# Performance work log

Hardware: AMD Instinct MI355X
Metric: run time of the kernel (lower is better)

Reference implementation:

```python
import jax, jax.numpy as jnp
import numpy as np
import math

B, I, O = 512, 512, 512
MEXHAT_NORM = 2.0 / (math.sqrt(3.0) * math.pi ** 0.25)
BN_EPS = 1e-5


def setup_inputs() -> dict:
    key = jax.random.key(0)
    kx, kw = jax.random.split(key, 2)
    x = jax.random.normal(kx, (B, I), dtype=jnp.float32)
    scale = jnp.ones((I, O), dtype=jnp.float32)
    bias = jnp.zeros((I, O), dtype=jnp.float32)
    # kaiming_uniform_ with a=sqrt(5): bound = sqrt(6 / ((1 + a^2) * fan_in)) = 1/sqrt(fan_in)
    bound = 1.0 / math.sqrt(I)
    weight = jax.random.uniform(kw, (I, O), dtype=jnp.float32, minval=-bound, maxval=bound)
    # BatchNorm1d affine params
    gamma = jnp.ones((O,), dtype=jnp.float32)
    beta = jnp.zeros((O,), dtype=jnp.float32)
    return {"x": x, "scale": scale, "bias": bias, "weight": weight,
            "gamma": gamma, "beta": beta}


def _mexhat_kan(x, scale, bias, weight):
    # x: (B, I); scale/bias/weight: (I, O)
    t = (x[:, :, None] - bias[None, :, :]) / scale[None, :, :]      # (B, I, O)
    t2 = t * t
    wav = MEXHAT_NORM * (t2 - 1.0) * jnp.exp(-0.5 * t2)             # Mexican hat
    return jnp.einsum('bio,io->bo', wav, weight)                    # reduce over in_features


def _batchnorm_train(y, gamma, beta):
    # BatchNorm1d in training mode: biased batch statistics over the batch dim
    mean = jnp.mean(y, axis=0)
    var = jnp.mean((y - mean) ** 2, axis=0)
    return (y - mean) * jax.lax.rsqrt(var + BN_EPS) * gamma + beta


def reference(x, scale, bias, weight, gamma, beta):
    y = _mexhat_kan(x, scale, bias, weight)   # (B, O)
    return _batchnorm_train(y, gamma, beta)
```

## Files before the change

kernel.cpp:

```cpp
#include <hip/hip_runtime.h>
#include <math.h>

#define B_ 512
#define I_ 512
#define O_ 512
#define BO_ (B_*O_)

#define TB 64
#define TO 16
#define KI 16
#define ZN 8
#define NIZ (I_/ZN)
#define NCHZ (NIZ/KI)
#define LXS (TB + 4)

#define SQH    0.84932180028801904f
#define MN_   (-1.2023679775792928f)
#define NN_   (-0.86732507058407750f)
#define NORM_  (0.86732507058407750f)
#define K_EXP  (-0.72134752044448170f)
#define BN_EPS (1e-5f)
#define NCH (I_/KI)

#if defined(__has_builtin)
#if __has_builtin(__builtin_amdgcn_exp2f)
#define EXP2F(v) __builtin_amdgcn_exp2f(v)
#endif
#endif
#ifndef EXP2F
#define EXP2F(v) exp2f(v)
#endif

__global__ __launch_bounds__(256) void kanZ(
    const float* __restrict__ x, const float* __restrict__ scale,
    const float* __restrict__ bias, const float* __restrict__ weight,
    float* __restrict__ pY)
{
    __shared__ float Lx[KI][LXS];
    __shared__ float Lp[KI][TO][4];

    const int fid = blockIdx.x;
    const int xcd = fid & 7;
    const int seq = fid >> 3;
    const int ot  = xcd * 4 + (seq & 3);
    const int by  = (seq >> 2) & 7;
    const int iz  = seq >> 5;

    const int o0 = ot * TO;
    const int b0 = by * TB;
    const int z0 = iz * NIZ;

    const int t   = threadIdx.x;
    const int to  = t & (TO - 1);
    const int tb4 = t >> 4;
    const int lb  = t >> 2;
    const int lq  = t & 3;
    const int li  = t >> 4;
    const int lo  = t & 15;

    float acc0 = 0.f, acc1 = 0.f, acc2 = 0.f, acc3 = 0.f;

    for (int ch = 0; ch < NCHZ; ++ch) {
        const int i0 = z0 + ch * KI;
        const float4 xv = *reinterpret_cast<const float4*>(
            &x[(size_t)(b0 + lb) * I_ + i0 + lq * 4]);
        const int pidx = (i0 + li) * O_ + o0 + lo;
        const float sc = scale[pidx];
        const float bi = bias[pidx];
        const float w  = weight[pidx];

        __syncthreads();
        Lx[lq * 4 + 0][lb] = xv.x;
        Lx[lq * 4 + 1][lb] = xv.y;
        Lx[lq * 4 + 2][lb] = xv.z;
        Lx[lq * 4 + 3][lb] = xv.w;
        const float c = SQH * __builtin_amdgcn_rcpf(sc);
        Lp[li][lo][0] = c;
        Lp[li][lo][1] = -bi * c;
        Lp[li][lo][2] = MN_ * w;
        Lp[li][lo][3] = NN_ * w;
        __syncthreads();

        #pragma unroll
        for (int ii = 0; ii < KI; ++ii) {
            const float4 p  = *reinterpret_cast<const float4*>(&Lp[ii][to][0]);
            const float4 x4 = *reinterpret_cast<const float4*>(&Lx[ii][tb4 * 4]);
            {
                const float h  = fmaf(x4.x, p.x, p.y);
                const float un = -h * h;
                const float e  = EXP2F(un);
                const float gg = fmaf(un, p.z, p.w);
                acc0 = fmaf(gg, e, acc0);
            }
            {
                const float h  = fmaf(x4.y, p.x, p.y);
                const float un = -h * h;
                const float e  = EXP2F(un);
                const float gg = fmaf(un, p.z, p.w);
                acc1 = fmaf(gg, e, acc1);
            }
            {
                const float h  = fmaf(x4.z, p.x, p.y);
                const float un = -h * h;
                const float e  = EXP2F(un);
                const float gg = fmaf(un, p.z, p.w);
                acc2 = fmaf(gg, e, acc2);
            }
            {
                const float h  = fmaf(x4.w, p.x, p.y);
                const float un = -h * h;
                const float e  = EXP2F(un);
                const float gg = fmaf(un, p.z, p.w);
                acc3 = fmaf(gg, e, acc3);
            }
        }
    }

    const size_t base = ((size_t)iz * B_ + b0 + tb4 * 4) * O_ + o0 + to;
    pY[base + 0 * O_] = acc0;
    pY[base + 1 * O_] = acc1;
    pY[base + 2 * O_] = acc2;
    pY[base + 3 * O_] = acc3;
}

__global__ __launch_bounds__(256) void comb_bn8(
    const float* __restrict__ pY,
    const float* __restrict__ gamma, const float* __restrict__ beta,
    float* __restrict__ y)
{
    __shared__ float Ws[4][8];
    __shared__ float Ac[8];

    const int bid = blockIdx.x;
    const int o4  = (bid & 7) * 64 + (bid >> 3) * 4;
    const int t   = threadIdx.x;

    float4 v[2];
    float sx = 0.f, sy = 0.f, sz = 0.f, sw = 0.f;
    float qx = 0.f, qy = 0.f, qz = 0.f, qw = 0.f;
    #pragma unroll
    for (int r = 0; r < 2; ++r) {
        const int b = t + 256 * r;
        const size_t base = (size_t)b * O_ + o4;
        float4 a = *reinterpret_cast<const float4*>(&pY[base]);
        #pragma unroll
        for (int z = 1; z < ZN; ++z) {
            const float4 p = *reinterpret_cast<const float4*>(&pY[(size_t)z * BO_ + base]);
            a.x += p.x; a.y += p.y; a.z += p.z; a.w += p.w;
        }
        v[r] = a;
        sx += a.x; sy += a.y; sz += a.z; sw += a.w;
        qx += a.x * a.x; qy += a.y * a.y; qz += a.z * a.z; qw += a.w * a.w;
    }

    #pragma unroll
    for (int m = 1; m < 64; m <<= 1) {
        sx += __shfl_xor(sx, m); sy += __shfl_xor(sy, m);
        sz += __shfl_xor(sz, m); sw += __shfl_xor(sw, m);
        qx += __shfl_xor(qx, m); qy += __shfl_xor(qy, m);
        qz += __shfl_xor(qz, m); qw += __shfl_xor(qw, m);
    }
    if ((t & 63) == 0) {
        const int wv = t >> 6;
        Ws[wv][0] = sx; Ws[wv][1] = sy; Ws[wv][2] = sz; Ws[wv][3] = sw;
        Ws[wv][4] = qx; Ws[wv][5] = qy; Ws[wv][6] = qz; Ws[wv][7] = qw;
    }
    __syncthreads();
    if (t < 4) {
        const float s  = Ws[0][t]     + Ws[1][t]     + Ws[2][t]     + Ws[3][t];
        const float q  = Ws[0][t + 4] + Ws[1][t + 4] + Ws[2][t + 4] + Ws[3][t + 4];
        const float mean = s * (1.0f / B_);
        const float var  = q * (1.0f / B_) - mean * mean;
        const float inv  = rsqrtf(var + BN_EPS);
        const float a = gamma[o4 + t] * inv;
        Ac[t]     = a;
        Ac[t + 4] = fmaf(-mean, a, beta[o4 + t]);
    }
    __syncthreads();

    const float4 a4 = *reinterpret_cast<const float4*>(&Ac[0]);
    const float4 c4 = *reinterpret_cast<const float4*>(&Ac[4]);
    #pragma unroll
    for (int r = 0; r < 2; ++r) {
        const int b = t + 256 * r;
        float4 o;
        o.x = fmaf(v[r].x, a4.x, c4.x);
        o.y = fmaf(v[r].y, a4.y, c4.y);
        o.z = fmaf(v[r].z, a4.z, c4.z);
        o.w = fmaf(v[r].w, a4.w, c4.w);
        *reinterpret_cast<float4*>(&y[(size_t)b * O_ + o4]) = o;
    }
}

__global__ __launch_bounds__(256) void kan_main(
    const float* __restrict__ x, const float* __restrict__ scale,
    const float* __restrict__ bias, const float* __restrict__ weight,
    float* __restrict__ y, float* __restrict__ psum, float* __restrict__ psumsq)
{
    __shared__ float LxF[KI][LXS];
    __shared__ float Lp[KI][TO][4];
    __shared__ float Rs[2][TB/4][TO];

    const int t   = threadIdx.x;
    const int to  = t & (TO - 1);
    const int tb4 = t >> 4;
    const int o0  = blockIdx.x * TO;
    const int b0  = blockIdx.y * TB;
    const int lb = t >> 2;
    const int lq = t & 3;
    const int li = t >> 4;
    const int lo = t & 15;

    float acc0 = 0.f, acc1 = 0.f, acc2 = 0.f, acc3 = 0.f;

    for (int ch = 0; ch < NCH; ++ch) {
        const int i0 = ch * KI;
        const float4 xv = *reinterpret_cast<const float4*>(&x[(b0 + lb) * I_ + i0 + lq * 4]);
        const int pidx = (i0 + li) * O_ + o0 + lo;
        const float sc = scale[pidx];
        const float bi = bias[pidx];
        const float w  = weight[pidx];

        __syncthreads();
        LxF[lq * 4 + 0][lb] = xv.x;
        LxF[lq * 4 + 1][lb] = xv.y;
        LxF[lq * 4 + 2][lb] = xv.z;
        LxF[lq * 4 + 3][lb] = xv.w;
        const float c = SQH * __builtin_amdgcn_rcpf(sc);
        Lp[li][lo][0] = c;
        Lp[li][lo][1] = -bi * c;
        Lp[li][lo][2] = MN_ * w;
        Lp[li][lo][3] = NN_ * w;
        __syncthreads();

        #pragma unroll
        for (int ii = 0; ii < KI; ++ii) {
            const float4 p  = *reinterpret_cast<const float4*>(&Lp[ii][to][0]);
            const float4 xx = *reinterpret_cast<const float4*>(&LxF[ii][tb4 * 4]);
            {
                const float h  = fmaf(xx.x, p.x, p.y);
                const float un = -h * h;
                const float e  = EXP2F(un);
                const float gg = fmaf(un, p.z, p.w);
                acc0 = fmaf(gg, e, acc0);
            }
            {
                const float h  = fmaf(xx.y, p.x, p.y);
                const float un = -h * h;
                const float e  = EXP2F(un);
                const float gg = fmaf(un, p.z, p.w);
                acc1 = fmaf(gg, e, acc1);
            }
            {
                const float h  = fmaf(xx.z, p.x, p.y);
                const float un = -h * h;
                const float e  = EXP2F(un);
                const float gg = fmaf(un, p.z, p.w);
                acc2 = fmaf(gg, e, acc2);
            }
            {
                const float h  = fmaf(xx.w, p.x, p.y);
                const float un = -h * h;
                const float e  = EXP2F(un);
                const float gg = fmaf(un, p.z, p.w);
                acc3 = fmaf(gg, e, acc3);
            }
        }
    }

    const int brow = b0 + tb4 * 4;
    y[(brow + 0) * O_ + o0 + to] = acc0;
    y[(brow + 1) * O_ + o0 + to] = acc1;
    y[(brow + 2) * O_ + o0 + to] = acc2;
    y[(brow + 3) * O_ + o0 + to] = acc3;

    Rs[0][tb4][to] = acc0 + acc1 + acc2 + acc3;
    Rs[1][tb4][to] = acc0 * acc0 + acc1 * acc1 + acc2 * acc2 + acc3 * acc3;
    __syncthreads();
    if (t < TO) {
        float s = 0.f, s2 = 0.f;
        #pragma unroll
        for (int k = 0; k < TB / 4; ++k) {
            s  += Rs[0][k][t];
            s2 += Rs[1][k][t];
        }
        psum  [blockIdx.y * O_ + o0 + t] = s;
        psumsq[blockIdx.y * O_ + o0 + t] = s2;
    }
}

__global__ __launch_bounds__(256) void bn_apply(
    const float* __restrict__ psum, const float* __restrict__ psumsq,
    const float* __restrict__ gamma, const float* __restrict__ beta,
    float* __restrict__ y)
{
    const int o = blockIdx.x * 256 + threadIdx.x;
    float s = 0.f, s2 = 0.f;
    #pragma unroll
    for (int k = 0; k < B_ / TB; ++k) {
        s  += psum  [k * O_ + o];
        s2 += psumsq[k * O_ + o];
    }
    const float mean = s * (1.0f / B_);
    const float var  = s2 * (1.0f / B_) - mean * mean;
    const float inv  = rsqrtf(var + BN_EPS);
    const float a = gamma[o] * inv;
    const float c = fmaf(-mean, a, beta[o]);

    const int bstart = blockIdx.y * 16;
    #pragma unroll
    for (int b = bstart; b < bstart + 16; ++b) {
        const int idx = b * O_ + o;
        y[idx] = fmaf(y[idx], a, c);
    }
}


extern "C" void kernel_launch(void* const* d_in, const int* in_sizes, int n_in,
                              void* d_out, int out_size, void* d_ws, size_t ws_size,
                              hipStream_t stream) {
    const float* x      = (const float*)d_in[0];
    const float* scale  = (const float*)d_in[1];
    const float* bias   = (const float*)d_in[2];
    const float* weight = (const float*)d_in[3];
    const float* gamma  = (const float*)d_in[4];
    const float* beta   = (const float*)d_in[5];
    float* out = (float*)d_out;

    const size_t pY_b = (size_t)ZN * BO_ * sizeof(float);

    if (ws_size >= pY_b) {
        float* pY = (float*)d_ws;
        kanZ<<<32 * 8 * 8, 256, 0, stream>>>(x, scale, bias, weight, pY);
        comb_bn8<<<O_ / 4, 256, 0, stream>>>(pY, gamma, beta, out);
    } else {
        float* psum   = (float*)d_ws;
        float* psumsq = psum + (B_ / TB) * O_;

        dim3 g1(O_ / TO, B_ / TB);
        kan_main<<<g1, 256, 0, stream>>>(x, scale, bias, weight, out, psum, psumsq);

        dim3 g2(O_ / 256, B_ / 16);
        bn_apply<<<g2, 256, 0, stream>>>(psum, psumsq, gamma, beta, out);
    }
}
```

Baseline: 32.97 us.

## Prepack per-(i,o) coefficients and transposed x, stream tiles via LDS DMA

Adds a pre-pass kernel that folds scale, bias and weight into a packed float4 of coefficients per (i,o) and transposes x. The main kernel then double-buffers these tiles into shared memory with global_load_lds DMA, so the inner loop does fewer arithmetic ops and loads overlap with compute. In exchange it adds an extra kernel launch and about 5 MB of extra workspace traffic to write and re-read the packed data, and the new path depends on the builtin being available and on a large enough workspace.

New measurement: 33.00 us. Within noise of the previous version (+0.1%).

```diff
diff --git a/kernel.cpp b/kernel.cpp
--- a/kernel.cpp
+++ b/kernel.cpp
@@ -5,6 +5,7 @@
 #define I_ 512
 #define O_ 512
 #define BO_ (B_*O_)
+#define IO_ (I_*O_)
 
 #define TB 64
 #define TO 16
@@ -18,7 +19,6 @@
 #define MN_   (-1.2023679775792928f)
 #define NN_   (-0.86732507058407750f)
 #define NORM_  (0.86732507058407750f)
-#define K_EXP  (-0.72134752044448170f)
 #define BN_EPS (1e-5f)
 #define NCH (I_/KI)
 
@@ -26,9 +26,150 @@
 #if __has_builtin(__builtin_amdgcn_exp2f)
 #define EXP2F(v) __builtin_amdgcn_exp2f(v)
 #endif
+#if __has_builtin(__builtin_amdgcn_global_load_lds)
+#define HAVE_DMA 1
+#endif
 #endif
 #ifndef EXP2F
 #define EXP2F(v) exp2f(v)
+#endif
+
+#ifdef HAVE_DMA
+__device__ __forceinline__ void dma16(const void* g, void* l) {
+    __builtin_amdgcn_global_load_lds(
+        (const __attribute__((address_space(1))) void*)g,
+        (__attribute__((address_space(3))) void*)l, 16, 0, 0);
+}
+#endif
+
+__global__ __launch_bounds__(256) void pack_px(
+    const float* __restrict__ x, const float* __restrict__ scale,
+    const float* __restrict__ bias, const float* __restrict__ weight,
+    float4* __restrict__ pp, float* __restrict__ xT)
+{
+    const int bid = blockIdx.x;
+    const int t   = threadIdx.x;
+
+    if (bid < IO_ / 256) {
+        const int g = bid * 256 + t;
+        const float sc = scale[g];
+        const float bi = bias[g];
+        const float w  = weight[g];
+        const float c  = SQH * __builtin_amdgcn_rcpf(sc);
+        pp[g] = make_float4(c, -bi * c, MN_ * w, NN_ * w);
+    } else {
+        __shared__ float T[64][68];
+        const int tile = bid - IO_ / 256;
+        const int i0 = (tile & 7) * 64;
+        const int b0 = (tile >> 3) * 64;
+        const int r  = t >> 4;
+        const int c4 = (t & 15) * 4;
+        #pragma unroll
+        for (int p = 0; p < 4; ++p) {
+            const int b = b0 + r + p * 16;
+            const float4 v = *reinterpret_cast<const float4*>(&x[(size_t)b * I_ + i0 + c4]);
+            T[c4 + 0][r + p * 16] = v.x;
+            T[c4 + 1][r + p * 16] = v.y;
+            T[c4 + 2][r + p * 16] = v.z;
+            T[c4 + 3][r + p * 16] = v.w;
+        }
+        __syncthreads();
+        #pragma unroll
+        for (int p = 0; p < 4; ++p) {
+            const int il = r + p * 16;
+            const float4 v = *reinterpret_cast<const float4*>(&T[il][c4]);
+            *reinterpret_cast<float4*>(&xT[(size_t)(i0 + il) * B_ + b0 + c4]) = v;
+        }
+    }
+}
+
+#ifdef HAVE_DMA
+__global__ __launch_bounds__(256) void kanD(
+    const float4* __restrict__ pp, const float* __restrict__ xT,
+    float* __restrict__ pY)
+{
+    __shared__ float4 Lp[2][KI][TO];
+    __shared__ float  Lx[2][KI][TB];
+
+    const int fid = blockIdx.x;
+    const int xcd = fid & 7;
+    const int seq = fid >> 3;
+    const int ot  = xcd * 4 + (seq & 3);
+    const int by  = (seq >> 2) & 7;
+    const int iz  = seq >> 5;
+
+    const int o0 = ot * TO;
+    const int b0 = by * TB;
+    const int z0 = iz * NIZ;
+
+    const int t   = threadIdx.x;
+    const int to  = t & (TO - 1);
+    const int tb4 = t >> 4;
+    const int wv  = t >> 6;
+    const int si  = t >> 4;
+    const int sq  = t & 15;
+
+    float acc0 = 0.f, acc1 = 0.f, acc2 = 0.f, acc3 = 0.f;
+
+#define STAGE(BUF, CH)                                                       \
+    {                                                                        \
+        const int i0_ = z0 + (CH) * KI;                                      \
+        dma16(&pp[(size_t)(i0_ + si) * O_ + o0 + sq],                        \
+              ((float*)&Lp[BUF][0][0]) + wv * 256);                          \
+        dma16(&xT[(size_t)(i0_ + si) * B_ + b0 + sq * 4],                    \
+              ((float*)&Lx[BUF][0][0]) + wv * 256);                          \
+    }
+
+    STAGE(0, 0);
+    __syncthreads();
+
+    #pragma unroll
+    for (int ch = 0; ch < NCHZ; ++ch) {
+        const int cur = ch & 1;
+        if (ch + 1 < NCHZ) STAGE(cur ^ 1, ch + 1);
+        #pragma unroll
+        for (int ii = 0; ii < KI; ++ii) {
+            const float4 p  = Lp[cur][ii][to];
+            const float4 x4 = *reinterpret_cast<const float4*>(&Lx[cur][ii][tb4 * 4]);
+            {
+                const float h  = fmaf(x4.x, p.x, p.y);
+                const float un = -h * h;
+                const float e  = EXP2F(un);
+                const float gg = fmaf(un, p.z, p.w);
+                acc0 = fmaf(gg, e, acc0);
+            }
+            {
+                const float h  = fmaf(x4.y, p.x, p.y);
+                const float un = -h * h;
+                const float e  = EXP2F(un);
+                const float gg = fmaf(un, p.z, p.w);
+                acc1 = fmaf(gg, e, acc1);
+            }
+            {
+                const float h  = fmaf(x4.z, p.x, p.y);
+                const float un = -h * h;
+                const float e  = EXP2F(un);
+                const float gg = fmaf(un, p.z, p.w);
+                acc2 = fmaf(gg, e, acc2);
+            }
+            {
+                const float h  = fmaf(x4.w, p.x, p.y);
+                const float un = -h * h;
+                const float e  = EXP2F(un);
+                const float gg = fmaf(un, p.z, p.w);
+                acc3 = fmaf(gg, e, acc3);
+            }
+        }
+        __syncthreads();
+    }
+#undef STAGE
+
+    const size_t base = ((size_t)iz * B_ + b0 + tb4 * 4) * O_ + o0 + to;
+    pY[base + 0 * O_] = acc0;
+    pY[base + 1 * O_] = acc1;
+    pY[base + 2 * O_] = acc2;
+    pY[base + 3 * O_] = acc3;
+}
 #endif
 
 __global__ __launch_bounds__(256) void kanZ(
@@ -327,8 +468,23 @@
     const float* beta   = (const float*)d_in[5];
     float* out = (float*)d_out;
 
-    const size_t pY_b = (size_t)ZN * BO_ * sizeof(float);
-
+    const size_t pY_b   = (size_t)ZN * BO_ * sizeof(float);
+    const size_t pp_b   = (size_t)IO_ * sizeof(float4);
+    const size_t xT_b   = (size_t)B_ * I_ * sizeof(float);
+    const size_t needD  = pY_b + pp_b + xT_b;
+
+#ifdef HAVE_DMA
+    if (ws_size >= needD) {
+        float*  pY = (float*)d_ws;
+        float4* pp = (float4*)((char*)d_ws + pY_b);
+        float*  xT = (float*)((char*)d_ws + pY_b + pp_b);
+
+        pack_px<<<IO_ / 256 + 64, 256, 0, stream>>>(x, scale, bias, weight, pp, xT);
+        kanD<<<32 * 8 * 8, 256, 0, stream>>>(pp, xT, pY);
+        comb_bn8<<<O_ / 4, 256, 0, stream>>>(pY, gamma, beta, out);
+        return;
+    }
+#endif
     if (ws_size >= pY_b) {
         float* pY = (float*)d_ws;
         kanZ<<<32 * 8 * 8, 256, 0, stream>>>(x, scale, bias, weight, pY);
```

## Precompute packed params and transposed x, use LDS DMA with 32-way split-I

Applied to the files above, without the earlier changes.

Adds a pre-pass kernel that packs scale/bias/weight into float4 coefficients and transposes x. The main kernel then loads tiles straight into LDS with global_load_lds DMA and computes a 64x64 output tile over a 16-wide slice of I, with a 32-way split. This removes per-chunk reciprocal and packing work plus register staging from the hot kernel. In exchange it adds an extra launch, writes and reads a 32x partial-sum buffer (32 MB) in the combine kernel, and needs a much larger workspace. The old fallback path without a workspace is removed.

After: 33.05 us. No clear change (+0.2%).

```diff
diff --git a/kernel.cpp b/kernel.cpp
--- a/kernel.cpp
+++ b/kernel.cpp
@@ -5,6 +5,10 @@
 #define I_ 512
 #define O_ 512
 #define BO_ (B_*O_)
+#define IO_ (I_*O_)
+
+#define ZR 32
+#define KIR 16
 
 #define TB 64
 #define TO 16
@@ -13,22 +17,154 @@
 #define NIZ (I_/ZN)
 #define NCHZ (NIZ/KI)
 #define LXS (TB + 4)
+#define NCH (I_/KI)
 
 #define SQH    0.84932180028801904f
 #define MN_   (-1.2023679775792928f)
 #define NN_   (-0.86732507058407750f)
-#define NORM_  (0.86732507058407750f)
-#define K_EXP  (-0.72134752044448170f)
 #define BN_EPS (1e-5f)
-#define NCH (I_/KI)
 
 #if defined(__has_builtin)
 #if __has_builtin(__builtin_amdgcn_exp2f)
 #define EXP2F(v) __builtin_amdgcn_exp2f(v)
 #endif
+#if __has_builtin(__builtin_amdgcn_global_load_lds)
+#define HAVE_DMA 1
+#endif
 #endif
 #ifndef EXP2F
 #define EXP2F(v) exp2f(v)
+#endif
+
+#ifdef HAVE_DMA
+__device__ __forceinline__ void dma16(const void* g, void* l) {
+    __builtin_amdgcn_global_load_lds(
+        (const __attribute__((address_space(1))) void*)g,
+        (__attribute__((address_space(3))) void*)l, 16, 0, 0);
+}
+#endif
+
+__global__ __launch_bounds__(256) void pack_px(
+    const float* __restrict__ x, const float* __restrict__ scale,
+    const float* __restrict__ bias, const float* __restrict__ weight,
+    float4* __restrict__ pp, float* __restrict__ xT)
+{
+    const int bid = blockIdx.x;
+    const int t   = threadIdx.x;
+
+    if (bid < IO_ / 256) {
+        const int g = bid * 256 + t;
+        const float sc = scale[g];
+        const float bi = bias[g];
+        const float w  = weight[g];
+        const float c  = SQH * __builtin_amdgcn_rcpf(sc);
+        pp[g] = make_float4(c, -bi * c, MN_ * w, NN_ * w);
+    } else {
+        __shared__ float T[64][68];
+        const int tile = bid - IO_ / 256;
+        const int i0 = (tile & 7) * 64;
+        const int b0 = (tile >> 3) * 64;
+        const int r  = t >> 4;
+        const int c4 = (t & 15) * 4;
+        #pragma unroll
+        for (int p = 0; p < 4; ++p) {
+            const int b = b0 + r + p * 16;
+            const float4 v = *reinterpret_cast<const float4*>(&x[(size_t)b * I_ + i0 + c4]);
+            T[c4 + 0][r + p * 16] = v.x;
+            T[c4 + 1][r + p * 16] = v.y;
+            T[c4 + 2][r + p * 16] = v.z;
+            T[c4 + 3][r + p * 16] = v.w;
+        }
+        __syncthreads();
+        #pragma unroll
+        for (int p = 0; p < 4; ++p) {
+            const int il = r + p * 16;
+            const float4 v = *reinterpret_cast<const float4*>(&T[il][c4]);
+            *reinterpret_cast<float4*>(&xT[(size_t)(i0 + il) * B_ + b0 + c4]) = v;
+        }
+    }
+}
+
+#ifdef HAVE_DMA
+__global__ __launch_bounds__(256) void kanR(
+    const float4* __restrict__ pp, const float* __restrict__ xT,
+    float* __restrict__ pY)
+{
+    __shared__ float4 Lp[KIR][64];
+    __shared__ float  Lx[KIR][64];
+
+    const int fid  = blockIdx.x;
+    const int ot   = fid & 7;
+    const int rest = fid >> 3;
+    const int bt   = rest & 7;
+    const int iz   = rest >> 3;
+
+    const int o0 = ot * 64;
+    const int b0 = bt * 64;
+    const int i0 = iz * KIR;
+
+    const int t  = threadIdx.x;
+    const int oq = t & 15;
+    const int bq = t >> 4;
+    const int wv = t >> 6;
+    const int l  = t & 63;
+
+    #pragma unroll
+    for (int k = 0; k < 4; ++k) {
+        dma16(&pp[(size_t)(i0 + wv * 4 + k) * O_ + o0 + l],
+              (char*)&Lp[0][0] + wv * 4096 + k * 1024);
+    }
+    dma16(&xT[(size_t)(i0 + wv * 4 + (l >> 4)) * B_ + b0 + (l & 15) * 4],
+          (char*)&Lx[0][0] + wv * 1024);
+
+    __syncthreads();
+
+    float4 acc0 = {0,0,0,0}, acc1 = {0,0,0,0}, acc2 = {0,0,0,0}, acc3 = {0,0,0,0};
+
+#define EVQ(xs, A)                                                           \
+    {                                                                        \
+        { const float h  = fmaf((xs), p0.x, p0.y);                           \
+          const float un = -h * h;                                           \
+          const float e  = EXP2F(un);                                        \
+          const float gg = fmaf(un, p0.z, p0.w);                             \
+          A.x = fmaf(gg, e, A.x); }                                          \
+        { const float h  = fmaf((xs), p1.x, p1.y);                           \
+          const float un = -h * h;                                           \
+          const float e  = EXP2F(un);                                        \
+          const float gg = fmaf(un, p1.z, p1.w);                             \
+          A.y = fmaf(gg, e, A.y); }                                          \
+        { const float h  = fmaf((xs), p2.x, p2.y);                           \
+          const float un = -h * h;                                           \
+          const float e  = EXP2F(un);                                        \
+          const float gg = fmaf(un, p2.z, p2.w);                             \
+          A.z = fmaf(gg, e, A.z); }                                          \
+        { const float h  = fmaf((xs), p3.x, p3.y);                           \
+          const float un = -h * h;                                           \
+          const float e  = EXP2F(un);                                        \
+          const float gg = fmaf(un, p3.z, p3.w);                             \
+          A.w = fmaf(gg, e, A.w); }                                          \
+    }
+
+    #pragma unroll 4
+    for (int ii = 0; ii < KIR; ++ii) {
+        const float4 x4 = *reinterpret_cast<const float4*>(&Lx[ii][bq * 4]);
+        const float4 p0 = Lp[ii][oq * 4 + 0];
+        const float4 p1 = Lp[ii][oq * 4 + 1];
+        const float4 p2 = Lp[ii][oq * 4 + 2];
+        const float4 p3 = Lp[ii][oq * 4 + 3];
+        EVQ(x4.x, acc0);
+        EVQ(x4.y, acc1);
+        EVQ(x4.z, acc2);
+        EVQ(x4.w, acc3);
+    }
+#undef EVQ
+
+    const size_t base = ((size_t)iz * B_ + b0 + bq * 4) * O_ + o0 + oq * 4;
+    *reinterpret_cast<float4*>(&pY[base + 0 * O_]) = acc0;
+    *reinterpret_cast<float4*>(&pY[base + 1 * O_]) = acc1;
+    *reinterpret_cast<float4*>(&pY[base + 2 * O_]) = acc2;
+    *reinterpret_cast<float4*>(&pY[base + 3 * O_]) = acc3;
+}
 #endif
 
 __global__ __launch_bounds__(256) void kanZ(
@@ -123,7 +259,8 @@
     pY[base + 3 * O_] = acc3;
 }
 
-__global__ __launch_bounds__(256) void comb_bn8(
+template <int NZ>
+__global__ __launch_bounds__(256) void comb_bn(
     const float* __restrict__ pY,
     const float* __restrict__ gamma, const float* __restrict__ beta,
     float* __restrict__ y)
@@ -144,7 +281,7 @@
         const size_t base = (size_t)b * O_ + o4;
         float4 a = *reinterpret_cast<const float4*>(&pY[base]);
         #pragma unroll
-        for (int z = 1; z < ZN; ++z) {
+        for (int z = 1; z < NZ; ++z) {
             const float4 p = *reinterpret_cast<const float4*>(&pY[(size_t)z * BO_ + base]);
             a.x += p.x; a.y += p.y; a.z += p.z; a.w += p.w;
         }
@@ -192,129 +329,6 @@
     }
 }
 
-__global__ __launch_bounds__(256) void kan_main(
-    const float* __restrict__ x, const float* __restrict__ scale,
-    const float* __restrict__ bias, const float* __restrict__ weight,
-    float* __restrict__ y, float* __restrict__ psum, float* __restrict__ psumsq)
-{
-    __shared__ float LxF[KI][LXS];
-    __shared__ float Lp[KI][TO][4];
-    __shared__ float Rs[2][TB/4][TO];
-
-    const int t   = threadIdx.x;
-    const int to  = t & (TO - 1);
-    const int tb4 = t >> 4;
-    const int o0  = blockIdx.x * TO;
-    const int b0  = blockIdx.y * TB;
-    const int lb = t >> 2;
-    const int lq = t & 3;
-    const int li = t >> 4;
-    const int lo = t & 15;
-
-    float acc0 = 0.f, acc1 = 0.f, acc2 = 0.f, acc3 = 0.f;
-
-    for (int ch = 0; ch < NCH; ++ch) {
-        const int i0 = ch * KI;
-        const float4 xv = *reinterpret_cast<const float4*>(&x[(b0 + lb) * I_ + i0 + lq * 4]);
-        const int pidx = (i0 + li) * O_ + o0 + lo;
-        const float sc = scale[pidx];
-        const float bi = bias[pidx];
-        const float w  = weight[pidx];
-
-        __syncthreads();
-        LxF[lq * 4 + 0][lb] = xv.x;
-        LxF[lq * 4 + 1][lb] = xv.y;
-        LxF[lq * 4 + 2][lb] = xv.z;
-        LxF[lq * 4 + 3][lb] = xv.w;
-        const float c = SQH * __builtin_amdgcn_rcpf(sc);
-        Lp[li][lo][0] = c;
-        Lp[li][lo][1] = -bi * c;
-        Lp[li][lo][2] = MN_ * w;
-        Lp[li][lo][3] = NN_ * w;
-        __syncthreads();
-
-        #pragma unroll
-        for (int ii = 0; ii < KI; ++ii) {
-            const float4 p  = *reinterpret_cast<const float4*>(&Lp[ii][to][0]);
-            const float4 xx = *reinterpret_cast<const float4*>(&LxF[ii][tb4 * 4]);
-            {
-                const float h  = fmaf(xx.x, p.x, p.y);
-                const float un = -h * h;
-                const float e  = EXP2F(un);
-                const float gg = fmaf(un, p.z, p.w);
-                acc0 = fmaf(gg, e, acc0);
-            }
-            {
-                const float h  = fmaf(xx.y, p.x, p.y);
-                const float un = -h * h;
-                const float e  = EXP2F(un);
-                const float gg = fmaf(un, p.z, p.w);
-                acc1 = fmaf(gg, e, acc1);
-            }
-            {
-                const float h  = fmaf(xx.z, p.x, p.y);
-                const float un = -h * h;
-                const float e  = EXP2F(un);
-                const float gg = fmaf(un, p.z, p.w);
-                acc2 = fmaf(gg, e, acc2);
-            }
-            {
-                const float h  = fmaf(xx.w, p.x, p.y);
-                const float un = -h * h;
-                const float e  = EXP2F(un);
-                const float gg = fmaf(un, p.z, p.w);
-                acc3 = fmaf(gg, e, acc3);
-            }
-        }
-    }
-
-    const int brow = b0 + tb4 * 4;
-    y[(brow + 0) * O_ + o0 + to] = acc0;
-    y[(brow + 1) * O_ + o0 + to] = acc1;
-    y[(brow + 2) * O_ + o0 + to] = acc2;
-    y[(brow + 3) * O_ + o0 + to] = acc3;
-
-    Rs[0][tb4][to] = acc0 + acc1 + acc2 + acc3;
-    Rs[1][tb4][to] = acc0 * acc0 + acc1 * acc1 + acc2 * acc2 + acc3 * acc3;
-    __syncthreads();
-    if (t < TO) {
-        float s = 0.f, s2 = 0.f;
-        #pragma unroll
-        for (int k = 0; k < TB / 4; ++k) {
-            s  += Rs[0][k][t];
-            s2 += Rs[1][k][t];
-        }
-        psum  [blockIdx.y * O_ + o0 + t] = s;
-        psumsq[blockIdx.y * O_ + o0 + t] = s2;
-    }
-}
-
-__global__ __launch_bounds__(256) void bn_apply(
-    const float* __restrict__ psum, const float* __restrict__ psumsq,
-    const float* __restrict__ gamma, const float* __restrict__ beta,
-    float* __restrict__ y)
-{
-    const int o = blockIdx.x * 256 + threadIdx.x;
-    float s = 0.f, s2 = 0.f;
-    #pragma unroll
-    for (int k = 0; k < B_ / TB; ++k) {
-        s  += psum  [k * O_ + o];
-        s2 += psumsq[k * O_ + o];
-    }
-    const float mean = s * (1.0f / B_);
-    const float var  = s2 * (1.0f / B_) - mean * mean;
-    const float inv  = rsqrtf(var + BN_EPS);
-    const float a = gamma[o] * inv;
-    const float c = fmaf(-mean, a, beta[o]);
-
-    const int bstart = blockIdx.y * 16;
-    #pragma unroll
-    for (int b = bstart; b < bstart + 16; ++b) {
-        const int idx = b * O_ + o;
-        y[idx] = fmaf(y[idx], a, c);
-    }
-}
-
 
 extern "C" void kernel_launch(void* const* d_in, const int* in_sizes, int n_in,
                               void* d_out, int out_size, void* d_ws, size_t ws_size,
@@ -327,20 +341,27 @@
     const float* beta   = (const float*)d_in[5];
     float* out = (float*)d_out;
 
-    const size_t pY_b = (size_t)ZN * BO_ * sizeof(float);
-
-    if (ws_size >= pY_b) {
+    const size_t pYR_b = (size_t)ZR * BO_ * sizeof(float);
+    const size_t pp_b  = (size_t)IO_ * sizeof(float4);
+    const size_t xT_b  = (size_t)B_ * I_ * sizeof(float);
+    const size_t needR = pYR_b + pp_b + xT_b;
+    const size_t pYZ_b = (size_t)ZN * BO_ * sizeof(float);
+
+#ifdef HAVE_DMA
+    if (ws_size >= needR) {
+        float*  pY = (float*)d_ws;
+        float4* pp = (float4*)((char*)d_ws + pYR_b);
+        float*  xT = (float*)((char*)d_ws + pYR_b + pp_b);
+
+        pack_px<<<IO_ / 256 + 64, 256, 0, stream>>>(x, scale, bias, weight, pp, xT);
+        kanR<<<8 * 8 * ZR, 256, 0, stream>>>(pp, xT, pY);
+        comb_bn<ZR><<<O_ / 4, 256, 0, stream>>>(pY, gamma, beta, out);
+        return;
+    }
+#endif
+    if (ws_size >= pYZ_b) {
         float* pY = (float*)d_ws;
         kanZ<<<32 * 8 * 8, 256, 0, stream>>>(x, scale, bias, weight, pY);
-        comb_bn8<<<O_ / 4, 256, 0, stream>>>(pY, gamma, beta, out);
-    } else {
-        float* psum   = (float*)d_ws;
-        float* psumsq = psum + (B_ / TB) * O_;
-
-        dim3 g1(O_ / TO, B_ / TB);
-        kan_main<<<g1, 256, 0, stream>>>(x, scale, bias, weight, out, psum, psumsq);
-
-        dim3 g2(O_ / 256, B_ / 16);
-        bn_apply<<<g2, 256, 0, stream>>>(psum, psumsq, gamma, beta, out);
-    }
-}
+        comb_bn<ZN><<<O_ / 4, 256, 0, stream>>>(pY, gamma, beta, out);
+    }
+}
```
